# Kernel optimization log

Hardware: AMD Instinct MI355X
Metric: run time of the kernel (lower is better)

The kernel has to match this reference:

```python
import jax, jax.numpy as jnp
import numpy as np

N = 2048      # total nodes across all graphs
G = 16        # number of graphs
IN = 16       # input_dim
D = 256       # hidden_dim (d_model)
NH = 8        # num_heads
HD = D // NH  # head_dim
FF = 4 * D    # dim_feedforward
L = 4         # num_layers
LAT = 32      # latent_dim
BH = D // 2   # beta_head hidden
LN_EPS = 1e-5


def setup_inputs() -> dict:
    key = jax.random.key(0)
    ks = jax.random.split(key, 32)

    def w(k, shape, fan_in):
        return jax.random.normal(k, shape, jnp.float32) * (1.0 / np.sqrt(fan_in))

    inp = {
        "x": jax.random.normal(ks[0], (N, IN), jnp.float32),
        "coords": jax.random.normal(ks[1], (N, 3), jnp.float32),
        "batch": jnp.sort(jax.random.randint(ks[2], (N,), 0, G)).astype(jnp.int32),
        # input projection
        "Wi": w(ks[3], (IN, D), IN), "bi": jnp.zeros((D,), jnp.float32),
        # per-layer transformer params, stacked on leading layer dim
        "qkv_w": w(ks[4], (L, D, 3 * D), D), "qkv_b": jnp.zeros((L, 3 * D), jnp.float32),
        "out_w": w(ks[5], (L, D, D), D),     "out_b": jnp.zeros((L, D), jnp.float32),
        "ff1_w": w(ks[6], (L, D, FF), D),    "ff1_b": jnp.zeros((L, FF), jnp.float32),
        "ff2_w": w(ks[7], (L, FF, D), FF),   "ff2_b": jnp.zeros((L, D), jnp.float32),
        "ln1_s": jnp.ones((L, D), jnp.float32), "ln1_b": jnp.zeros((L, D), jnp.float32),
        "ln2_s": jnp.ones((L, D), jnp.float32), "ln2_b": jnp.zeros((L, D), jnp.float32),
        # heads
        "lat_w": w(ks[8], (D, LAT), D), "lat_b": jnp.zeros((LAT,), jnp.float32),
        "b1_w": w(ks[9], (D, BH), D),   "b1_b": jnp.zeros((BH,), jnp.float32),
        "b2_w": w(ks[10], (BH, 1), BH), "b2_b": jnp.zeros((1,), jnp.float32),
    }
    return inp


def _layer_norm(h, s, b):
    m = jnp.mean(h, axis=-1, keepdims=True)
    v = jnp.mean(jnp.square(h - m), axis=-1, keepdims=True)
    return (h - m) * jax.lax.rsqrt(v + LN_EPS) * s + b


def _forward(x, batch, Wi, bi, qkv_w, qkv_b, out_w, out_b, ff1_w, ff1_b,
             ff2_w, ff2_b, ln1_s, ln1_b, ln2_s, ln2_b, lat_w, lat_b,
             b1_w, b1_b, b2_w, b2_b):
    n = x.shape[0]
    h = x @ Wi + bi  # [N, D]
    # the per-graph python loop in torch == block-diagonal attention mask
    attn_bias = jnp.where(batch[:, None] == batch[None, :], 0.0, -1e9).astype(h.dtype)  # [N, N]
    scale = 1.0 / np.sqrt(HD)
    for l in range(L):
        qkv = h @ qkv_w[l] + qkv_b[l]                 # [N, 3D]
        q, k, v = jnp.split(qkv, 3, axis=-1)
        q = q.reshape(n, NH, HD)
        k = k.reshape(n, NH, HD)
        v = v.reshape(n, NH, HD)
        scores = jnp.einsum('nhd,mhd->hnm', q, k) * scale + attn_bias[None]  # [H, N, N]
        a = jax.nn.softmax(scores, axis=-1)
        o = jnp.einsum('hnm,mhd->nhd', a, v).reshape(n, D)
        o = o @ out_w[l] + out_b[l]
        h = _layer_norm(h + o, ln1_s[l], ln1_b[l])     # post-norm (torch default)
        f = jax.nn.relu(h @ ff1_w[l] + ff1_b[l]) @ ff2_w[l] + ff2_b[l]
        h = _layer_norm(h + f, ln2_s[l], ln2_b[l])
    lat = h @ lat_w + lat_b                            # [N, LAT]
    norm = jnp.maximum(jnp.linalg.norm(lat, axis=-1, keepdims=True), 1e-12)
    lat = lat / norm * np.sqrt(LAT)
    beta = jax.nn.sigmoid(jax.nn.relu(h @ b1_w + b1_b) @ b2_w + b2_b)  # [N, 1]
    beta = jnp.clip(beta, 1e-6, 1.0 - 1e-6)
    return beta, lat


def reference(x, coords, batch, Wi, bi, qkv_w, qkv_b, out_w, out_b,
              ff1_w, ff1_b, ff2_w, ff2_b, ln1_s, ln1_b, ln2_s, ln2_b,
              lat_w, lat_b, b1_w, b1_b, b2_w, b2_b):
    # coords is accepted (signature fidelity) but unused in the original forward
    del coords
    return _forward(x, batch, Wi, bi, qkv_w, qkv_b, out_w, out_b, ff1_w, ff1_b,
                    ff2_w, ff2_b, ln1_s, ln1_b, ln2_s, ln2_b, lat_w, lat_b,
                    b1_w, b1_b, b2_w, b2_b)
```

## Files before the change

kernel.cpp:

```cpp
#include <hip/hip_runtime.h>
#include <hip/hip_bf16.h>

typedef __attribute__((ext_vector_type(8))) short bf16x8;
typedef __attribute__((ext_vector_type(4))) float f32x4;

__device__ inline float wave_sum64(float v) {
#pragma unroll
  for (int m = 32; m >= 1; m >>= 1) v += __shfl_xor(v, m, 64);
  return v;
}
__device__ inline ushort f2bf(float f) {
  uint u = __float_as_uint(f);
  return (ushort)((u + 0x7FFFu + ((u >> 16) & 1u)) >> 16);
}

__global__ __launch_bounds__(256) void pack_weights(
    const float* __restrict__ qkv_w, const float* __restrict__ out_w,
    const float* __restrict__ ff1_w, const float* __restrict__ ff2_w,
    const float* __restrict__ b1_w, const float* __restrict__ lat_w,
    short* __restrict__ qkv_t, short* __restrict__ out_t,
    short* __restrict__ ff1_t, short* __restrict__ ff2_t,
    short* __restrict__ b1_t, short* __restrict__ lat_t,
    const int* __restrict__ batch, int* __restrict__ starts) {
  int t = blockIdx.x;
  if (t == 3112) {
    for (int i = threadIdx.x; i < 2048; i += 256) {
      int b = batch[i];
      if (i == 0) {
        for (int g = 0; g <= b; ++g) starts[g] = 0;
      } else {
        int bp = batch[i - 1];
        for (int g = bp + 1; g <= b; ++g) starts[g] = i;
      }
      if (i == 2047) {
        for (int g = b + 1; g <= 16; ++g) starts[g] = 2048;
      }
    }
    return;
  }
  const float* src;
  short* dst;
  int Kd, Nd, rem;
  if (t < 768) {
    int l = t / 192; rem = t % 192; Kd = 256; Nd = 768;
    src = qkv_w + (size_t)l * Kd * Nd; dst = qkv_t + (size_t)l * Nd * Kd;
  } else if (t < 1024) {
    t -= 768; int l = t / 64; rem = t % 64; Kd = 256; Nd = 256;
    src = out_w + (size_t)l * Kd * Nd; dst = out_t + (size_t)l * Nd * Kd;
  } else if (t < 2048) {
    t -= 1024; int l = t / 256; rem = t % 256; Kd = 256; Nd = 1024;
    src = ff1_w + (size_t)l * Kd * Nd; dst = ff1_t + (size_t)l * Nd * Kd;
  } else if (t < 3072) {
    t -= 2048; int l = t / 256; rem = t % 256; Kd = 1024; Nd = 256;
    src = ff2_w + (size_t)l * Kd * Nd; dst = ff2_t + (size_t)l * Nd * Kd;
  } else if (t < 3104) {
    rem = t - 3072; Kd = 256; Nd = 128; src = b1_w; dst = b1_t;
  } else {
    rem = t - 3104; Kd = 256; Nd = 32; src = lat_w; dst = lat_t;
  }
  const int ntn = Nd / 32;
  const int kt = rem / ntn, nt = rem % ntn;

  __shared__ float tile[32][33];
  const int tx = threadIdx.x & 31, ty = threadIdx.x >> 5;
#pragma unroll
  for (int r = 0; r < 4; ++r) {
    int k = kt * 32 + ty + r * 8;
    tile[ty + r * 8][tx] = src[(size_t)k * Nd + nt * 32 + tx];
  }
  __syncthreads();
#pragma unroll
  for (int r = 0; r < 4; ++r) {
    int n = nt * 32 + ty + r * 8;
    dst[(size_t)n * Kd + kt * 32 + tx] = (short)f2bf(tile[tx][ty + r * 8]);
  }
}

__global__ __launch_bounds__(256) void inproj_kernel(
    const float* __restrict__ x, const float* __restrict__ Wi,
    const float* __restrict__ bi, float* __restrict__ h, short* __restrict__ hb) {
  __shared__ float xs[16];
  const int i = blockIdx.x, j = threadIdx.x;
  if (j < 16) xs[j] = x[(size_t)i * 16 + j];
  __syncthreads();
  float acc = bi[j];
#pragma unroll
  for (int k = 0; k < 16; ++k) acc += xs[k] * Wi[k * 256 + j];
  h[(size_t)i * 256 + j] = acc;
  hb[(size_t)i * 256 + j] = (short)f2bf(acc);
}

template <int ACT, int OUTBF>
__global__ __launch_bounds__(256) void gemm_bf16(
    const short* __restrict__ A, const short* __restrict__ Bt,
    const float* __restrict__ bias, float* __restrict__ Cf, short* __restrict__ Cb,
    int M, int N, int K, int kpb) {
  __shared__ short As[64 * 128];
  __shared__ short Bs[64 * 128];

  const int t = threadIdx.x;
  const int bm = blockIdx.y, bn = blockIdx.x, bz = blockIdx.z;
  const int srow = t >> 2, sq = t & 3;
  const int lane = t & 63, wid = t >> 6;
  const int wr = wid >> 1, wc = wid & 1;
  const int fr = lane & 15, fs = lane >> 4;
  const int rx = srow & 7;

  f32x4 acc[2][2];
#pragma unroll
  for (int m = 0; m < 2; ++m)
#pragma unroll
    for (int n = 0; n < 2; ++n) acc[m][n] = (f32x4){0.f, 0.f, 0.f, 0.f};

  const int kbase = bz * kpb;
  const short* ap = A + (size_t)(bm * 64 + srow) * K + kbase;
  const int ng = bn * 64 + srow;
  const short* bp = Bt + (size_t)ng * K + kbase;

  const int ar0 = wr * 32 + fr, ar1 = ar0 + 16;
  const int bc0 = wc * 32 + fr, bc1 = bc0 + 16;

  for (int k0 = 0; k0 < kpb; k0 += 128) {
    bf16x8 av[4], bv[4];
#pragma unroll
    for (int i = 0; i < 4; ++i) av[i] = *(const bf16x8*)(ap + k0 + (sq * 4 + i) * 8);
    if (ng < N) {
#pragma unroll
      for (int i = 0; i < 4; ++i) bv[i] = *(const bf16x8*)(bp + k0 + (sq * 4 + i) * 8);
    } else {
#pragma unroll
      for (int i = 0; i < 4; ++i) bv[i] = (bf16x8){0, 0, 0, 0, 0, 0, 0, 0};
    }
    __syncthreads();
#pragma unroll
    for (int i = 0; i < 4; ++i) {
      const int s = sq * 4 + i;
      *(bf16x8*)(As + srow * 128 + ((s ^ rx) * 8)) = av[i];
      *(bf16x8*)(Bs + srow * 128 + ((s ^ rx) * 8)) = bv[i];
    }
    __syncthreads();

#pragma unroll
    for (int ks = 0; ks < 4; ++ks) {
      const int u = ks * 4 + fs;
      bf16x8 a0 = *(const bf16x8*)(As + ar0 * 128 + ((u ^ (ar0 & 7)) * 8));
      bf16x8 a1 = *(const bf16x8*)(As + ar1 * 128 + ((u ^ (ar1 & 7)) * 8));
      bf16x8 b0 = *(const bf16x8*)(Bs + bc0 * 128 + ((u ^ (bc0 & 7)) * 8));
      bf16x8 b1 = *(const bf16x8*)(Bs + bc1 * 128 + ((u ^ (bc1 & 7)) * 8));
      acc[0][0] = __builtin_amdgcn_mfma_f32_16x16x32_bf16(a0, b0, acc[0][0], 0, 0, 0);
      acc[0][1] = __builtin_amdgcn_mfma_f32_16x16x32_bf16(a0, b1, acc[0][1], 0, 0, 0);
      acc[1][0] = __builtin_amdgcn_mfma_f32_16x16x32_bf16(a1, b0, acc[1][0], 0, 0, 0);
      acc[1][1] = __builtin_amdgcn_mfma_f32_16x16x32_bf16(a1, b1, acc[1][1], 0, 0, 0);
    }
  }

#pragma unroll
  for (int n = 0; n < 2; ++n) {
    const int col = bn * 64 + wc * 32 + n * 16 + fr;
    if (col >= N) continue;
    const float bvv = (bz == 0) ? bias[col] : 0.f;
#pragma unroll
    for (int m = 0; m < 2; ++m) {
      const int rbase = bm * 64 + wr * 32 + m * 16 + fs * 4;
#pragma unroll
      for (int j = 0; j < 4; ++j) {
        float v = acc[m][n][j] + bvv;
        if (ACT == 1) v = fmaxf(v, 0.f);
        if (OUTBF) {
          Cb[(size_t)(rbase + j) * N + col] = (short)f2bf(v);
        } else {
          Cf[(size_t)(bz * M + rbase + j) * N + col] = v;
        }
      }
    }
  }
}

__global__ __launch_bounds__(256) void attn_mfma(
    const short* __restrict__ qkv, const int* __restrict__ starts,
    short* __restrict__ out) {
  const int g = blockIdx.x >> 3;
  const int h = blockIdx.x & 7;
  const int t = threadIdx.x;
  const int lane = t & 63, w = t >> 6;
  const int fr = lane & 15, fs = lane >> 4;
  const int js = starts[g], je = starts[g + 1];
  const int Lg = je - js;

  __shared__ __align__(16) short Ks[128][40];
  __shared__ __align__(16) short Vt[32][128];
  __shared__ __align__(16) short Ps[4][16][128];

  const float scale = 0.17677669529663687f;
  const bf16x8 bz8 = (bf16x8){0, 0, 0, 0, 0, 0, 0, 0};

  bf16x8 qf[4];
  f32x4 oa[4][2];
  float mrow[4][4], lrow[4][4];
#pragma unroll
  for (int tt = 0; tt < 4; ++tt) {
    const int q0 = js + (w + tt * 4) * 16;
    const int row = min(q0 + fr, 2047);
    qf[tt] = *(const bf16x8*)(qkv + (size_t)row * 768 + h * 32 + fs * 8);
    oa[tt][0] = (f32x4){0.f, 0.f, 0.f, 0.f};
    oa[tt][1] = (f32x4){0.f, 0.f, 0.f, 0.f};
#pragma unroll
    for (int j = 0; j < 4; ++j) { mrow[tt][j] = -3.0e38f; lrow[tt][j] = 0.f; }
  }

  const int nch = (Lg + 127) >> 7;
  for (int c = 0; c < nch; ++c) {
    const int c0 = js + (c << 7);
    __syncthreads();
    {
      const int r = t >> 1, half = t & 1;
      const int jr = c0 + r;
      bf16x8 k0 = bz8, k1 = bz8, v0 = bz8, v1 = bz8;
      if (jr < je) {
        const short* kp = qkv + (size_t)jr * 768 + 256 + h * 32 + half * 16;
        k0 = *(const bf16x8*)kp;
        k1 = *(const bf16x8*)(kp + 8);
        v0 = *(const bf16x8*)(kp + 256);
        v1 = *(const bf16x8*)(kp + 264);
      }
      *(bf16x8*)&Ks[r][half * 16] = k0;
      *(bf16x8*)&Ks[r][half * 16 + 8] = k1;
#pragma unroll
      for (int i = 0; i < 8; ++i) {
        const int d0 = half * 16 + i;
        const int d1 = d0 + 8;
        Vt[d0][((((r >> 3) ^ (d0 & 7)) << 3) | (r & 7))] = v0[i];
        Vt[d1][((((r >> 3) ^ (d1 & 7)) << 3) | (r & 7))] = v1[i];
      }
    }
    __syncthreads();

#pragma unroll
    for (int tt = 0; tt < 4; ++tt) {
      if ((w + tt * 4) * 16 >= Lg) continue;
      f32x4 s[8];
#pragma unroll
      for (int jt = 0; jt < 8; ++jt) {
        const bf16x8 kf = *(const bf16x8*)&Ks[jt * 16 + fr][fs * 8];
        s[jt] = __builtin_amdgcn_mfma_f32_16x16x32_bf16(
            qf[tt], kf, (f32x4){0.f, 0.f, 0.f, 0.f}, 0, 0, 0);
      }
#pragma unroll
      for (int jt = 0; jt < 8; ++jt) {
        const bool valid = (c0 + jt * 16 + fr) < je;
#pragma unroll
        for (int j = 0; j < 4; ++j) s[jt][j] = valid ? s[jt][j] * scale : -3.0e38f;
      }
#pragma unroll
      for (int j = 0; j < 4; ++j) {
        float mx = s[0][j];
#pragma unroll
        for (int jt = 1; jt < 8; ++jt) mx = fmaxf(mx, s[jt][j]);
        mx = fmaxf(mx, __shfl_xor(mx, 1, 64));
        mx = fmaxf(mx, __shfl_xor(mx, 2, 64));
        mx = fmaxf(mx, __shfl_xor(mx, 4, 64));
        mx = fmaxf(mx, __shfl_xor(mx, 8, 64));
        const float mn = fmaxf(mrow[tt][j], mx);
        const float corr = __expf(mrow[tt][j] - mn);
        mrow[tt][j] = mn;
        float rs = 0.f;
#pragma unroll
        for (int jt = 0; jt < 8; ++jt) {
          const float p = __expf(s[jt][j] - mn);
          s[jt][j] = p;
          rs += p;
        }
        rs += __shfl_xor(rs, 1, 64);
        rs += __shfl_xor(rs, 2, 64);
        rs += __shfl_xor(rs, 4, 64);
        rs += __shfl_xor(rs, 8, 64);
        lrow[tt][j] = lrow[tt][j] * corr + rs;
        oa[tt][0][j] *= corr;
        oa[tt][1][j] *= corr;
      }
#pragma unroll
      for (int jt = 0; jt < 8; ++jt) {
#pragma unroll
        for (int j = 0; j < 4; ++j) {
          const int q = fs * 4 + j;
          Ps[w][q][((((jt * 2 + (fr >> 3)) ^ (q & 7)) << 3) | (fr & 7))] =
              (short)f2bf(s[jt][j]);
        }
      }
#pragma unroll
      for (int jq = 0; jq < 4; ++jq) {
        const int slot = ((jq * 4 + fs) ^ (fr & 7)) << 3;
        const bf16x8 pf = *(const bf16x8*)&Ps[w][fr][slot];
#pragma unroll
        for (int nt = 0; nt < 2; ++nt) {
          const bf16x8 vf = *(const bf16x8*)&Vt[nt * 16 + fr][slot];
          oa[tt][nt] = __builtin_amdgcn_mfma_f32_16x16x32_bf16(pf, vf, oa[tt][nt], 0, 0, 0);
        }
      }
    }
  }

#pragma unroll
  for (int tt = 0; tt < 4; ++tt) {
    if ((w + tt * 4) * 16 >= Lg) continue;
    const int q0 = js + (w + tt * 4) * 16;
#pragma unroll
    for (int j = 0; j < 4; ++j) {
      const int node = q0 + fs * 4 + j;
      if (node < je) {
        const float inv = 1.f / lrow[tt][j];
        out[(size_t)node * 256 + h * 32 + fr] = (short)f2bf(oa[tt][0][j] * inv);
        out[(size_t)node * 256 + h * 32 + 16 + fr] = (short)f2bf(oa[tt][1][j] * inv);
      }
    }
  }
}

template <int P>
__global__ __launch_bounds__(256) void ln_kernel(
    const float* __restrict__ base, const float* __restrict__ delta,
    const float* __restrict__ s, const float* __restrict__ b,
    float* __restrict__ outf, short* __restrict__ outb) {
  const int row = blockIdx.x * 4 + (threadIdx.x >> 6);
  const int lane = threadIdx.x & 63;
  const float4 xa = *(const float4*)(base + (size_t)row * 256 + lane * 4);
  float4 v = xa;
#pragma unroll
  for (int p = 0; p < P; ++p) {
    const float4 xb = *(const float4*)(delta + (size_t)(p * 2048 + row) * 256 + lane * 4);
    v.x += xb.x; v.y += xb.y; v.z += xb.z; v.w += xb.w;
  }
  float sum = v.x + v.y + v.z + v.w;
  sum = wave_sum64(sum);
  const float mean = sum * (1.f / 256.f);
  float4 d = make_float4(v.x - mean, v.y - mean, v.z - mean, v.w - mean);
  float sq = d.x * d.x + d.y * d.y + d.z * d.z + d.w * d.w;
  sq = wave_sum64(sq);
  const float rs = rsqrtf(sq * (1.f / 256.f) + 1e-5f);
  const float4 sv = *(const float4*)(s + lane * 4);
  const float4 bv = *(const float4*)(b + lane * 4);
  float4 o = make_float4(d.x * rs * sv.x + bv.x, d.y * rs * sv.y + bv.y,
                         d.z * rs * sv.z + bv.z, d.w * rs * sv.w + bv.w);
  *(float4*)(outf + (size_t)row * 256 + lane * 4) = o;
  short4 ob;
  ob.x = (short)f2bf(o.x); ob.y = (short)f2bf(o.y);
  ob.z = (short)f2bf(o.z); ob.w = (short)f2bf(o.w);
  *(short4*)(outb + (size_t)row * 256 + lane * 4) = ob;
}

__global__ __launch_bounds__(256) void lat_kernel(
    const short* __restrict__ A, const short* __restrict__ Bt,
    const float* __restrict__ bias, float* __restrict__ out) {
  __shared__ short As[64 * 128];
  __shared__ short Bs[64 * 128];
  const int t = threadIdx.x;
  const int bm = blockIdx.x;
  const int srow = t >> 2, sq = t & 3;
  const int lane = t & 63, w = t >> 6;
  const int fr = lane & 15, fs = lane >> 4;
  const int rx = srow & 7;

  f32x4 acc[2];
  acc[0] = (f32x4){0.f, 0.f, 0.f, 0.f};
  acc[1] = (f32x4){0.f, 0.f, 0.f, 0.f};

  const short* ap = A + (size_t)(bm * 64 + srow) * 256;
  const short* bp = Bt + (size_t)srow * 256;
  const int ar = w * 16 + fr;

  for (int k0 = 0; k0 < 256; k0 += 128) {
    bf16x8 av[4], bv[4];
#pragma unroll
    for (int i = 0; i < 4; ++i) av[i] = *(const bf16x8*)(ap + k0 + (sq * 4 + i) * 8);
    if (srow < 32) {
#pragma unroll
      for (int i = 0; i < 4; ++i) bv[i] = *(const bf16x8*)(bp + k0 + (sq * 4 + i) * 8);
    } else {
#pragma unroll
      for (int i = 0; i < 4; ++i) bv[i] = (bf16x8){0, 0, 0, 0, 0, 0, 0, 0};
    }
    __syncthreads();
#pragma unroll
    for (int i = 0; i < 4; ++i) {
      const int s = sq * 4 + i;
      *(bf16x8*)(As + srow * 128 + ((s ^ rx) * 8)) = av[i];
      *(bf16x8*)(Bs + srow * 128 + ((s ^ rx) * 8)) = bv[i];
    }
    __syncthreads();
#pragma unroll
    for (int ks = 0; ks < 4; ++ks) {
      const int u = ks * 4 + fs;
      bf16x8 a0 = *(const bf16x8*)(As + ar * 128 + ((u ^ (ar & 7)) * 8));
      bf16x8 b0 = *(const bf16x8*)(Bs + fr * 128 + ((u ^ (fr & 7)) * 8));
      bf16x8 b1 = *(const bf16x8*)(Bs + (16 + fr) * 128 + ((u ^ ((16 + fr) & 7)) * 8));
      acc[0] = __builtin_amdgcn_mfma_f32_16x16x32_bf16(a0, b0, acc[0], 0, 0, 0);
      acc[1] = __builtin_amdgcn_mfma_f32_16x16x32_bf16(a0, b1, acc[1], 0, 0, 0);
    }
  }

  const float b0v = bias[fr], b1v = bias[16 + fr];
#pragma unroll
  for (int j = 0; j < 4; ++j) {
    const int row = bm * 64 + w * 16 + fs * 4 + j;
    float v0 = acc[0][j] + b0v;
    float v1 = acc[1][j] + b1v;
    float ss = v0 * v0 + v1 * v1;
    ss += __shfl_xor(ss, 1, 64);
    ss += __shfl_xor(ss, 2, 64);
    ss += __shfl_xor(ss, 4, 64);
    ss += __shfl_xor(ss, 8, 64);
    const float inv = 5.656854249492381f / fmaxf(sqrtf(ss), 1e-12f);
    out[(size_t)row * 32 + fr] = v0 * inv;
    out[(size_t)row * 32 + 16 + fr] = v1 * inv;
  }
}

__global__ __launch_bounds__(256) void beta_kernel(
    const float* __restrict__ bh, const float* __restrict__ w,
    const float* __restrict__ b2b, float* __restrict__ beta) {
  const int row = blockIdx.x * 4 + (threadIdx.x >> 6);
  const int lane = threadIdx.x & 63;
  float p = bh[(size_t)row * 128 + lane] * w[lane] +
            bh[(size_t)row * 128 + 64 + lane] * w[64 + lane];
  p = wave_sum64(p);
  if (lane == 0) {
    float x = p + b2b[0];
    float sgm = 1.f / (1.f + __expf(-x));
    sgm = fminf(fmaxf(sgm, 1e-6f), 1.f - 1e-6f);
    beta[row] = sgm;
  }
}

extern "C" void kernel_launch(void* const* d_in, const int* in_sizes, int n_in,
                              void* d_out, int out_size, void* d_ws, size_t ws_size,
                              hipStream_t stream) {
  const int N = 2048, D = 256, FF = 1024, L = 4;

  const float* x     = (const float*)d_in[0];
  const int*   batch = (const int*)d_in[2];
  const float* Wi    = (const float*)d_in[3];
  const float* bi    = (const float*)d_in[4];
  const float* qkv_w = (const float*)d_in[5];
  const float* qkv_b = (const float*)d_in[6];
  const float* out_w = (const float*)d_in[7];
  const float* out_b = (const float*)d_in[8];
  const float* ff1_w = (const float*)d_in[9];
  const float* ff1_b = (const float*)d_in[10];
  const float* ff2_w = (const float*)d_in[11];
  const float* ff2_b = (const float*)d_in[12];
  const float* ln1_s = (const float*)d_in[13];
  const float* ln1_b = (const float*)d_in[14];
  const float* ln2_s = (const float*)d_in[15];
  const float* ln2_b = (const float*)d_in[16];
  const float* lat_w = (const float*)d_in[17];
  const float* lat_b = (const float*)d_in[18];
  const float* b1_w  = (const float*)d_in[19];
  const float* b1_b  = (const float*)d_in[20];
  const float* b2_w  = (const float*)d_in[21];
  const float* b2_b  = (const float*)d_in[22];

  float* ws = (float*)d_ws;
  float* h      = ws;
  float* tmp    = h + (size_t)N * D;
  float* bh     = tmp + (size_t)4 * N * D;
  int*  starts  = (int*)(bh + (size_t)N * 128);
  short* hb     = (short*)(starts + 32);
  short* qkvb   = hb + (size_t)N * D;
  short* attnb  = qkvb + (size_t)N * 3 * D;
  short* ffb    = attnb + (size_t)N * D;
  short* qkv_t  = ffb + (size_t)N * FF;
  short* out_t  = qkv_t + (size_t)L * 768 * 256;
  short* ff1_t  = out_t + (size_t)L * 256 * 256;
  short* ff2_t  = ff1_t + (size_t)L * 1024 * 256;
  short* b1_t   = ff2_t + (size_t)L * 256 * 1024;
  short* lat_t  = b1_t + (size_t)128 * 256;

  float* beta_out = (float*)d_out;
  float* lat_out  = beta_out + N;

  pack_weights<<<3113, 256, 0, stream>>>(qkv_w, out_w, ff1_w, ff2_w, b1_w, lat_w,
                                         qkv_t, out_t, ff1_t, ff2_t, b1_t, lat_t,
                                         batch, starts);
  inproj_kernel<<<N, 256, 0, stream>>>(x, Wi, bi, h, hb);

  for (int l = 0; l < L; ++l) {
    gemm_bf16<0, 1><<<dim3(12, 32, 1), 256, 0, stream>>>(
        hb, qkv_t + (size_t)l * 768 * 256, qkv_b + (size_t)l * 768,
        nullptr, qkvb, N, 768, 256, 256);
    attn_mfma<<<16 * 8, 256, 0, stream>>>(qkvb, starts, attnb);
    gemm_bf16<0, 0><<<dim3(4, 32, 2), 256, 0, stream>>>(
        attnb, out_t + (size_t)l * 256 * 256, out_b + (size_t)l * 256,
        tmp, nullptr, N, 256, 256, 128);
    ln_kernel<2><<<N / 4, 256, 0, stream>>>(h, tmp, ln1_s + (size_t)l * D,
                                            ln1_b + (size_t)l * D, h, hb);
    gemm_bf16<1, 1><<<dim3(16, 32, 1), 256, 0, stream>>>(
        hb, ff1_t + (size_t)l * FF * 256, ff1_b + (size_t)l * FF,
        nullptr, ffb, N, FF, 256, 256);
    gemm_bf16<0, 0><<<dim3(4, 32, 4), 256, 0, stream>>>(
        ffb, ff2_t + (size_t)l * 256 * FF, ff2_b + (size_t)l * 256,
        tmp, nullptr, N, 256, 1024, 256);
    ln_kernel<4><<<N / 4, 256, 0, stream>>>(h, tmp, ln2_s + (size_t)l * D,
                                            ln2_b + (size_t)l * D, h, hb);
  }

  lat_kernel<<<N / 64, 256, 0, stream>>>(hb, lat_t, lat_b, lat_out);
  gemm_bf16<1, 0><<<dim3(2, 32, 1), 256, 0, stream>>>(
      hb, b1_t, b1_b, bh, nullptr, N, 128, 256, 256);
  beta_kernel<<<N / 4, 256, 0, stream>>>(bh, b2_w, b2_b, beta_out);
}
```

Before: 213.4 us.

## Replace per-graph flash attention with per-wave query-tile attention using pre-transposed V

The attention kernel used to launch one block per (graph, head) and loop over 128-key chunks through LDS with online softmax. It now launches one wave per (16-query tile, head) from a host-free tile table built in pack_weights, and does a single-pass softmax over up to 256 keys held in registers. The QKV GEMM epilogue also writes V transposed to global memory, so the PV MFMA can read V directly without LDS staging. This spreads the work over many more waves and drops LDS traffic and barriers. In exchange it adds extra scattered stores in the GEMM epilogue, and it assumes graphs of at most about 256 nodes and a fixed meta buffer size.

Result: slower. 220.1 us (+3.1%).

```diff
diff --git a/kernel.cpp b/kernel.cpp
--- a/kernel.cpp
+++ b/kernel.cpp
@@ -21,7 +21,7 @@
     short* __restrict__ qkv_t, short* __restrict__ out_t,
     short* __restrict__ ff1_t, short* __restrict__ ff2_t,
     short* __restrict__ b1_t, short* __restrict__ lat_t,
-    const int* __restrict__ batch, int* __restrict__ starts) {
+    const int* __restrict__ batch, int* __restrict__ starts, int* __restrict__ meta) {
   int t = blockIdx.x;
   if (t == 3112) {
     for (int i = threadIdx.x; i < 2048; i += 256) {
@@ -35,6 +35,20 @@
       if (i == 2047) {
         for (int g = b + 1; g <= 16; ++g) starts[g] = 2048;
       }
+    }
+    __syncthreads();
+    if (threadIdx.x == 0) {
+      int nt = 0;
+      for (int g = 0; g < 16; ++g) {
+        const int js = starts[g], je = starts[g + 1];
+        for (int q0 = js; q0 < je; q0 += 16) {
+          meta[1 + nt * 3] = q0;
+          meta[2 + nt * 3] = js;
+          meta[3 + nt * 3] = je;
+          ++nt;
+        }
+      }
+      meta[0] = nt;
     }
     return;
   }
@@ -90,11 +104,11 @@
   hb[(size_t)i * 256 + j] = (short)f2bf(acc);
 }
 
-template <int ACT, int OUTBF>
+template <int ACT, int OUTBF, int VT>
 __global__ __launch_bounds__(256) void gemm_bf16(
     const short* __restrict__ A, const short* __restrict__ Bt,
     const float* __restrict__ bias, float* __restrict__ Cf, short* __restrict__ Cb,
-    int M, int N, int K, int kpb) {
+    short* __restrict__ vtg, int M, int N, int K, int kpb) {
   __shared__ short As[64 * 128];
   __shared__ short Bs[64 * 128];
 
@@ -167,7 +181,11 @@
         float v = acc[m][n][j] + bvv;
         if (ACT == 1) v = fmaxf(v, 0.f);
         if (OUTBF) {
-          Cb[(size_t)(rbase + j) * N + col] = (short)f2bf(v);
+          const short bfv = (short)f2bf(v);
+          Cb[(size_t)(rbase + j) * N + col] = bfv;
+          if (VT && col >= 512) {
+            vtg[(size_t)(col - 512) * 2048 + rbase + j] = bfv;
+          }
         } else {
           Cf[(size_t)(bz * M + rbase + j) * N + col] = v;
         }
@@ -176,142 +194,101 @@
   }
 }
 
-__global__ __launch_bounds__(256) void attn_mfma(
-    const short* __restrict__ qkv, const int* __restrict__ starts,
-    short* __restrict__ out) {
-  const int g = blockIdx.x >> 3;
-  const int h = blockIdx.x & 7;
-  const int t = threadIdx.x;
-  const int lane = t & 63, w = t >> 6;
+__global__ __launch_bounds__(256) void attn_direct(
+    const short* __restrict__ qkv, const short* __restrict__ vtg,
+    const int* __restrict__ meta, short* __restrict__ out) {
+  const int wid = blockIdx.x * 4 + (threadIdx.x >> 6);
+  const int tile = wid >> 3, h = wid & 7;
+  if (tile >= meta[0]) return;
+  const int lane = threadIdx.x & 63;
   const int fr = lane & 15, fs = lane >> 4;
-  const int js = starts[g], je = starts[g + 1];
-  const int Lg = je - js;
-
-  __shared__ __align__(16) short Ks[128][40];
-  __shared__ __align__(16) short Vt[32][128];
-  __shared__ __align__(16) short Ps[4][16][128];
-
+  const int q0 = meta[1 + tile * 3];
+  const int js = meta[2 + tile * 3];
+  const int je = meta[3 + tile * 3];
+  const int jbase = js & ~15;
+  const int njt = (je - jbase + 15) >> 4;
   const float scale = 0.17677669529663687f;
-  const bf16x8 bz8 = (bf16x8){0, 0, 0, 0, 0, 0, 0, 0};
-
-  bf16x8 qf[4];
-  f32x4 oa[4][2];
-  float mrow[4][4], lrow[4][4];
-#pragma unroll
-  for (int tt = 0; tt < 4; ++tt) {
-    const int q0 = js + (w + tt * 4) * 16;
-    const int row = min(q0 + fr, 2047);
-    qf[tt] = *(const bf16x8*)(qkv + (size_t)row * 768 + h * 32 + fs * 8);
-    oa[tt][0] = (f32x4){0.f, 0.f, 0.f, 0.f};
-    oa[tt][1] = (f32x4){0.f, 0.f, 0.f, 0.f};
-#pragma unroll
-    for (int j = 0; j < 4; ++j) { mrow[tt][j] = -3.0e38f; lrow[tt][j] = 0.f; }
-  }
-
-  const int nch = (Lg + 127) >> 7;
-  for (int c = 0; c < nch; ++c) {
-    const int c0 = js + (c << 7);
-    __syncthreads();
-    {
-      const int r = t >> 1, half = t & 1;
-      const int jr = c0 + r;
-      bf16x8 k0 = bz8, k1 = bz8, v0 = bz8, v1 = bz8;
-      if (jr < je) {
-        const short* kp = qkv + (size_t)jr * 768 + 256 + h * 32 + half * 16;
-        k0 = *(const bf16x8*)kp;
-        k1 = *(const bf16x8*)(kp + 8);
-        v0 = *(const bf16x8*)(kp + 256);
-        v1 = *(const bf16x8*)(kp + 264);
-      }
-      *(bf16x8*)&Ks[r][half * 16] = k0;
-      *(bf16x8*)&Ks[r][half * 16 + 8] = k1;
-#pragma unroll
-      for (int i = 0; i < 8; ++i) {
-        const int d0 = half * 16 + i;
-        const int d1 = d0 + 8;
-        Vt[d0][((((r >> 3) ^ (d0 & 7)) << 3) | (r & 7))] = v0[i];
-        Vt[d1][((((r >> 3) ^ (d1 & 7)) << 3) | (r & 7))] = v1[i];
-      }
-    }
-    __syncthreads();
-
-#pragma unroll
-    for (int tt = 0; tt < 4; ++tt) {
-      if ((w + tt * 4) * 16 >= Lg) continue;
-      f32x4 s[8];
-#pragma unroll
-      for (int jt = 0; jt < 8; ++jt) {
-        const bf16x8 kf = *(const bf16x8*)&Ks[jt * 16 + fr][fs * 8];
-        s[jt] = __builtin_amdgcn_mfma_f32_16x16x32_bf16(
-            qf[tt], kf, (f32x4){0.f, 0.f, 0.f, 0.f}, 0, 0, 0);
-      }
-#pragma unroll
-      for (int jt = 0; jt < 8; ++jt) {
-        const bool valid = (c0 + jt * 16 + fr) < je;
-#pragma unroll
-        for (int j = 0; j < 4; ++j) s[jt][j] = valid ? s[jt][j] * scale : -3.0e38f;
-      }
-#pragma unroll
-      for (int j = 0; j < 4; ++j) {
-        float mx = s[0][j];
-#pragma unroll
-        for (int jt = 1; jt < 8; ++jt) mx = fmaxf(mx, s[jt][j]);
-        mx = fmaxf(mx, __shfl_xor(mx, 1, 64));
-        mx = fmaxf(mx, __shfl_xor(mx, 2, 64));
-        mx = fmaxf(mx, __shfl_xor(mx, 4, 64));
-        mx = fmaxf(mx, __shfl_xor(mx, 8, 64));
-        const float mn = fmaxf(mrow[tt][j], mx);
-        const float corr = __expf(mrow[tt][j] - mn);
-        mrow[tt][j] = mn;
-        float rs = 0.f;
-#pragma unroll
-        for (int jt = 0; jt < 8; ++jt) {
-          const float p = __expf(s[jt][j] - mn);
-          s[jt][j] = p;
-          rs += p;
-        }
-        rs += __shfl_xor(rs, 1, 64);
-        rs += __shfl_xor(rs, 2, 64);
-        rs += __shfl_xor(rs, 4, 64);
-        rs += __shfl_xor(rs, 8, 64);
-        lrow[tt][j] = lrow[tt][j] * corr + rs;
-        oa[tt][0][j] *= corr;
-        oa[tt][1][j] *= corr;
-      }
-#pragma unroll
-      for (int jt = 0; jt < 8; ++jt) {
-#pragma unroll
-        for (int j = 0; j < 4; ++j) {
-          const int q = fs * 4 + j;
-          Ps[w][q][((((jt * 2 + (fr >> 3)) ^ (q & 7)) << 3) | (fr & 7))] =
-              (short)f2bf(s[jt][j]);
-        }
-      }
-#pragma unroll
-      for (int jq = 0; jq < 4; ++jq) {
-        const int slot = ((jq * 4 + fs) ^ (fr & 7)) << 3;
-        const bf16x8 pf = *(const bf16x8*)&Ps[w][fr][slot];
-#pragma unroll
-        for (int nt = 0; nt < 2; ++nt) {
-          const bf16x8 vf = *(const bf16x8*)&Vt[nt * 16 + fr][slot];
-          oa[tt][nt] = __builtin_amdgcn_mfma_f32_16x16x32_bf16(pf, vf, oa[tt][nt], 0, 0, 0);
-        }
-      }
-    }
-  }
-
-#pragma unroll
-  for (int tt = 0; tt < 4; ++tt) {
-    if ((w + tt * 4) * 16 >= Lg) continue;
-    const int q0 = js + (w + tt * 4) * 16;
-#pragma unroll
-    for (int j = 0; j < 4; ++j) {
-      const int node = q0 + fs * 4 + j;
-      if (node < je) {
-        const float inv = 1.f / lrow[tt][j];
-        out[(size_t)node * 256 + h * 32 + fr] = (short)f2bf(oa[tt][0][j] * inv);
-        out[(size_t)node * 256 + h * 32 + 16 + fr] = (short)f2bf(oa[tt][1][j] * inv);
-      }
+
+  const int qrow = min(q0 + fr, 2047);
+  const bf16x8 qf = *(const bf16x8*)(qkv + (size_t)qrow * 768 + h * 32 + fs * 8);
+  const int jeq = (q0 + fr < je) ? je : 0;
+
+  f32x4 s[16];
+#pragma unroll
+  for (int jt = 0; jt < 16; ++jt)
+    s[jt] = (f32x4){-3.0e38f, -3.0e38f, -3.0e38f, -3.0e38f};
+
+#pragma unroll
+  for (int jt = 0; jt < 16; ++jt) {
+    if (jt < njt) {
+      const int krow = min(jbase + jt * 16 + fr, 2047);
+      const bf16x8 kf = *(const bf16x8*)(qkv + (size_t)krow * 768 + 256 + h * 32 + fs * 8);
+      s[jt] = __builtin_amdgcn_mfma_f32_16x16x32_bf16(
+          kf, qf, (f32x4){0.f, 0.f, 0.f, 0.f}, 0, 0, 0);
+    }
+  }
+  float mx = -3.0e38f;
+#pragma unroll
+  for (int jt = 0; jt < 16; ++jt) {
+    if (jt < njt) {
+#pragma unroll
+      for (int jj = 0; jj < 4; ++jj) {
+        const int j = jbase + jt * 16 + fs * 4 + jj;
+        const bool valid = (j >= js) && (j < jeq);
+        s[jt][jj] = valid ? s[jt][jj] * scale : -3.0e38f;
+        mx = fmaxf(mx, s[jt][jj]);
+      }
+    }
+  }
+  mx = fmaxf(mx, __shfl_xor(mx, 16, 64));
+  mx = fmaxf(mx, __shfl_xor(mx, 32, 64));
+  float l = 0.f;
+#pragma unroll
+  for (int jt = 0; jt < 16; ++jt) {
+#pragma unroll
+    for (int jj = 0; jj < 4; ++jj) {
+      const float p = __expf(s[jt][jj] - mx);
+      s[jt][jj] = p;
+      l += p;
+    }
+  }
+  l += __shfl_xor(l, 16, 64);
+  l += __shfl_xor(l, 32, 64);
+
+  f32x4 oa[2];
+  oa[0] = (f32x4){0.f, 0.f, 0.f, 0.f};
+  oa[1] = (f32x4){0.f, 0.f, 0.f, 0.f};
+#pragma unroll
+  for (int p2 = 0; p2 < 8; ++p2) {
+    if (p2 * 2 < njt) {
+      bf16x8 pa;
+      pa[0] = (short)f2bf(s[p2 * 2][0]);     pa[1] = (short)f2bf(s[p2 * 2][1]);
+      pa[2] = (short)f2bf(s[p2 * 2][2]);     pa[3] = (short)f2bf(s[p2 * 2][3]);
+      pa[4] = (short)f2bf(s[p2 * 2 + 1][0]); pa[5] = (short)f2bf(s[p2 * 2 + 1][1]);
+      pa[6] = (short)f2bf(s[p2 * 2 + 1][2]); pa[7] = (short)f2bf(s[p2 * 2 + 1][3]);
+      const int jb0 = min(jbase + p2 * 32 + fs * 4, 2044);
+      const int jb1 = min(jbase + p2 * 32 + 16 + fs * 4, 2044);
+#pragma unroll
+      for (int nt = 0; nt < 2; ++nt) {
+        const short* vrow = vtg + (size_t)(h * 32 + nt * 16 + fr) * 2048;
+        const short4 v0 = *(const short4*)(vrow + jb0);
+        const short4 v1 = *(const short4*)(vrow + jb1);
+        bf16x8 vf;
+        vf[0] = v0.x; vf[1] = v0.y; vf[2] = v0.z; vf[3] = v0.w;
+        vf[4] = v1.x; vf[5] = v1.y; vf[6] = v1.z; vf[7] = v1.w;
+        oa[nt] = __builtin_amdgcn_mfma_f32_16x16x32_bf16(pa, vf, oa[nt], 0, 0, 0);
+      }
+    }
+  }
+
+#pragma unroll
+  for (int jj = 0; jj < 4; ++jj) {
+    const float lq = __shfl(l, fs * 4 + jj, 64);
+    const int node = q0 + fs * 4 + jj;
+    if (node < je) {
+      const float inv = 1.f / lq;
+      out[(size_t)node * 256 + h * 32 + fr] = (short)f2bf(oa[0][jj] * inv);
+      out[(size_t)node * 256 + h * 32 + 16 + fr] = (short)f2bf(oa[1][jj] * inv);
     }
   }
 }
@@ -464,11 +441,13 @@
   float* tmp    = h + (size_t)N * D;
   float* bh     = tmp + (size_t)4 * N * D;
   int*  starts  = (int*)(bh + (size_t)N * 128);
-  short* hb     = (short*)(starts + 32);
+  int*  meta    = starts + 32;
+  short* hb     = (short*)(meta + 448);
   short* qkvb   = hb + (size_t)N * D;
   short* attnb  = qkvb + (size_t)N * 3 * D;
   short* ffb    = attnb + (size_t)N * D;
-  short* qkv_t  = ffb + (size_t)N * FF;
+  short* vtg    = ffb + (size_t)N * FF;
+  short* qkv_t  = vtg + (size_t)256 * 2048;
   short* out_t  = qkv_t + (size_t)L * 768 * 256;
   short* ff1_t  = out_t + (size_t)L * 256 * 256;
   short* ff2_t  = ff1_t + (size_t)L * 1024 * 256;
@@ -480,31 +459,31 @@
 
   pack_weights<<<3113, 256, 0, stream>>>(qkv_w, out_w, ff1_w, ff2_w, b1_w, lat_w,
                                          qkv_t, out_t, ff1_t, ff2_t, b1_t, lat_t,
-                                         batch, starts);
+                                         batch, starts, meta);
   inproj_kernel<<<N, 256, 0, stream>>>(x, Wi, bi, h, hb);
 
   for (int l = 0; l < L; ++l) {
-    gemm_bf16<0, 1><<<dim3(12, 32, 1), 256, 0, stream>>>(
+    gemm_bf16<0, 1, 1><<<dim3(12, 32, 1), 256, 0, stream>>>(
         hb, qkv_t + (size_t)l * 768 * 256, qkv_b + (size_t)l * 768,
-        nullptr, qkvb, N, 768, 256, 256);
-    attn_mfma<<<16 * 8, 256, 0, stream>>>(qkvb, starts, attnb);
-    gemm_bf16<0, 0><<<dim3(4, 32, 2), 256, 0, stream>>>(
+        nullptr, qkvb, vtg, N, 768, 256, 256);
+    attn_direct<<<288, 256, 0, stream>>>(qkvb, vtg, meta, attnb);
+    gemm_bf16<0, 0, 0><<<dim3(4, 32, 2), 256, 0, stream>>>(
         attnb, out_t + (size_t)l * 256 * 256, out_b + (size_t)l * 256,
-        tmp, nullptr, N, 256, 256, 128);
+        tmp, nullptr, nullptr, N, 256, 256, 128);
     ln_kernel<2><<<N / 4, 256, 0, stream>>>(h, tmp, ln1_s + (size_t)l * D,
                                             ln1_b + (size_t)l * D, h, hb);
-    gemm_bf16<1, 1><<<dim3(16, 32, 1), 256, 0, stream>>>(
+    gemm_bf16<1, 1, 0><<<dim3(16, 32, 1), 256, 0, stream>>>(
         hb, ff1_t + (size_t)l * FF * 256, ff1_b + (size_t)l * FF,
-        nullptr, ffb, N, FF, 256, 256);
-    gemm_bf16<0, 0><<<dim3(4, 32, 4), 256, 0, stream>>>(
+        nullptr, ffb, nullptr, N, FF, 256, 256);
+    gemm_bf16<0, 0, 0><<<dim3(4, 32, 4), 256, 0, stream>>>(
         ffb, ff2_t + (size_t)l * 256 * FF, ff2_b + (size_t)l * 256,
-        tmp, nullptr, N, 256, 1024, 256);
+        tmp, nullptr, nullptr, N, 256, 1024, 256);
     ln_kernel<4><<<N / 4, 256, 0, stream>>>(h, tmp, ln2_s + (size_t)l * D,
                                             ln2_b + (size_t)l * D, h, hb);
   }
 
   lat_kernel<<<N / 64, 256, 0, stream>>>(hb, lat_t, lat_b, lat_out);
-  gemm_bf16<1, 0><<<dim3(2, 32, 1), 256, 0, stream>>>(
-      hb, b1_t, b1_b, bh, nullptr, N, 128, 256, 256);
+  gemm_bf16<1, 0, 0><<<dim3(2, 32, 1), 256, 0, stream>>>(
+      hb, b1_t, b1_b, bh, nullptr, nullptr, N, 128, 256, 256);
   beta_kernel<<<N / 4, 256, 0, stream>>>(bh, b2_w, b2_b, beta_out);
 }
```
